# Optimization experiments

Measured on AMD Instinct MI355X. Metric: run time of the kernel, lower is better.

## Reference

```python
import jax, jax.numpy as jnp
import numpy as np

B, T, R, V = 16, 512, 128, 64
HOURS = 24.0


def setup_inputs() -> dict:
    key = jax.random.key(0)
    k1, k2, k3, k4, k5 = jax.random.split(key, 5)
    x = jax.random.normal(k1, (B, T, V), dtype=jnp.float32)
    # observation mask in {0,1}
    m = (jax.random.uniform(k2, (B, T, V)) < 0.5).astype(jnp.float32)
    # irregular observation times in [0, HOURS), sorted per sample
    t = jnp.sort(jax.random.uniform(k3, (B, T), dtype=jnp.float32) * HOURS, axis=1)
    # hold-out mask (only used in reconstruction branch; kept for signature parity)
    h = (jax.random.uniform(k4, (B, T, V)) < 0.5).astype(jnp.float32)
    # learnable per-variable kernel bandwidth (pre-softplus), shape (1,1,1,V)
    kernel = jax.random.normal(k5, (1, 1, 1, V), dtype=jnp.float32) * 0.1
    # fixed reference time grid, shape (R,)
    ref_t = jnp.linspace(0.0, HOURS, R, dtype=jnp.float32)
    return {"x": x, "m": m, "t": t, "h": h, "kernel": kernel, "ref_t": ref_t}


def reference(x, m, t, h, kernel, ref_t):
    # squared time distances: (B, T, R)
    d2 = (t[:, :, None] - ref_t[None, None, :]) ** 2
    pos_kernel = jnp.log1p(jnp.exp(kernel))          # softplus, (1,1,1,V)
    w = pos_kernel * d2[:, :, :, None]               # (B, T, R, V)
    m4 = m[:, :, None, :]                            # (B, T, 1, V)
    x4 = x[:, :, None, :]
    # low-pass branch
    w_lp = jnp.exp(-w) * m4
    lambda_ = w_lp.sum(axis=1)                       # (B, R, V)
    sigma = (w_lp * x4).sum(axis=1) / jnp.maximum(lambda_, 1.0)
    # high-pass branch
    w_hp = jnp.exp(-10.0 * w) * m4
    lambda_hp = w_hp.sum(axis=1)
    gamma = (w_hp * x4).sum(axis=1) / jnp.maximum(lambda_hp, 1.0)
    return (sigma, lambda_, gamma)
```

## Files before the change

kernel.cpp:

```cpp
#include <hip/hip_runtime.h>
#include <hip/hip_bf16.h>

#define NB 16
#define NT 512
#define NR 128
#define NV 64
#define RG 4
#define NCH 8

__global__ __launch_bounds__(512) void interp_kernel(
    const float* __restrict__ x,
    const float* __restrict__ m,
    const float* __restrict__ t,
    const float* __restrict__ kern,
    const float* __restrict__ ref_t,
    float* __restrict__ out)
{
    __shared__ float ts[NT];
    __shared__ float red[NCH][4 * RG][NV];

    const int tid   = threadIdx.x;
    const int v     = tid & 63;
    const int chunk = tid >> 6;
    const int bid   = blockIdx.x;
    const int b     = bid >> 5;
    const int rg    = bid & 31;
    const int r0    = rg * RG;

    for (int i = tid; i < NT; i += 512) ts[i] = t[b * NT + i];

    const float kv  = kern[v];
    const float pk  = log1pf(__expf(kv));
    const float npk = -pk;

    float rt[RG];
#pragma unroll
    for (int j = 0; j < RG; ++j) rt[j] = ref_t[r0 + j];

    float lam[RG], sig[RG], lamh[RG], gam[RG];
#pragma unroll
    for (int j = 0; j < RG; ++j) { lam[j] = 0.f; sig[j] = 0.f; lamh[j] = 0.f; gam[j] = 0.f; }

    __syncthreads();

    const int t_base = chunk * (NT / NCH);
    const float* __restrict__ xrow = x + (size_t)b * NT * NV + v;
    const float* __restrict__ mrow = m + (size_t)b * NT * NV + v;

    for (int i = 0; i < NT / NCH; ++i) {
        const int tt   = t_base + i;
        const float tv = ts[tt];
        const float mv = mrow[(size_t)tt * NV];
        const float xv = xrow[(size_t)tt * NV];
        const float mx = mv * xv;
#pragma unroll
        for (int j = 0; j < RG; ++j) {
            const float dt  = tv - rt[j];
            const float wn  = npk * (dt * dt);
            const float e   = __expf(wn);
            const float e10 = __expf(10.0f * wn);
            lam[j]  = fmaf(e,   mv, lam[j]);
            sig[j]  = fmaf(e,   mx, sig[j]);
            lamh[j] = fmaf(e10, mv, lamh[j]);
            gam[j]  = fmaf(e10, mx, gam[j]);
        }
    }

#pragma unroll
    for (int j = 0; j < RG; ++j) {
        red[chunk][j * 4 + 0][v] = lam[j];
        red[chunk][j * 4 + 1][v] = sig[j];
        red[chunk][j * 4 + 2][v] = lamh[j];
        red[chunk][j * 4 + 3][v] = gam[j];
    }
    __syncthreads();

    if (chunk < RG) {
        const int jj = chunk;
        float flam = 0.f, fsig = 0.f, flamh = 0.f, fgam = 0.f;
#pragma unroll
        for (int c = 0; c < NCH; ++c) {
            flam  += red[c][jj * 4 + 0][v];
            fsig  += red[c][jj * 4 + 1][v];
            flamh += red[c][jj * 4 + 2][v];
            fgam  += red[c][jj * 4 + 3][v];
        }
        const float sigma = fsig / fmaxf(flam, 1.0f);
        const float gamma = fgam / fmaxf(flamh, 1.0f);

        const int r = r0 + jj;
        const size_t o = ((size_t)b * NR + r) * NV + v;
        out[o]                            = sigma;
        out[o + (size_t)NB * NR * NV]     = flam;
        out[o + (size_t)2 * NB * NR * NV] = gamma;
    }
}

extern "C" void kernel_launch(void* const* d_in, const int* in_sizes, int n_in,
                              void* d_out, int out_size, void* d_ws, size_t ws_size,
                              hipStream_t stream) {
    const float* x     = (const float*)d_in[0];
    const float* m     = (const float*)d_in[1];
    const float* t     = (const float*)d_in[2];
    const float* kern  = (const float*)d_in[4];
    const float* ref_t = (const float*)d_in[5];
    float* out = (float*)d_out;

    dim3 grid(NB * (NR / RG));
    dim3 block(512);
    interp_kernel<<<grid, block, 0, stream>>>(x, m, t, kern, ref_t, out);
}
```

Baseline: 89.70 us.

## Restrict time loop to window around reference points via binary search cutoff

```diff
diff --git a/kernel.cpp b/kernel.cpp
--- a/kernel.cpp
+++ b/kernel.cpp
@@ -1,5 +1,4 @@
 #include <hip/hip_runtime.h>
-#include <hip/hip_bf16.h>
 
 #define NB 16
 #define NT 512
@@ -7,6 +6,8 @@
 #define NV 64
 #define RG 4
 #define NCH 8
+
+#define CUT 12.0f
 
 __global__ __launch_bounds__(512) void interp_kernel(
     const float* __restrict__ x,
@@ -27,15 +28,23 @@
     const int rg    = bid & 31;
     const int r0    = rg * RG;
 
-    for (int i = tid; i < NT; i += 512) ts[i] = t[b * NT + i];
+    ts[tid] = t[b * NT + tid];
 
-    const float kv  = kern[v];
-    const float pk  = log1pf(__expf(kv));
-    const float npk = -pk;
+    const float kv   = kern[v];
+    const float pk   = log1pf(__expf(kv));
+    const float npk2 = -pk * 1.44269504088896f;
+
+    float pmin = pk;
+#pragma unroll
+    for (int off = 1; off < 64; off <<= 1)
+        pmin = fminf(pmin, __shfl_xor(pmin, off));
+    const float dmax = __fsqrt_rn(CUT / pmin);
 
     float rt[RG];
 #pragma unroll
     for (int j = 0; j < RG; ++j) rt[j] = ref_t[r0 + j];
+    const float wlo = rt[0]      - dmax;
+    const float whi = rt[RG - 1] + dmax;
 
     float lam[RG], sig[RG], lamh[RG], gam[RG];
 #pragma unroll
@@ -43,22 +52,30 @@
 
     __syncthreads();
 
-    const int t_base = chunk * (NT / NCH);
+    int lo, hi;
+    {
+        int l = 0, r = NT;
+        while (l < r) { int mid = (l + r) >> 1; if (ts[mid] < wlo) l = mid + 1; else r = mid; }
+        lo = l;
+        l = 0; r = NT;
+        while (l < r) { int mid = (l + r) >> 1; if (ts[mid] <= whi) l = mid + 1; else r = mid; }
+        hi = l;
+    }
+
     const float* __restrict__ xrow = x + (size_t)b * NT * NV + v;
     const float* __restrict__ mrow = m + (size_t)b * NT * NV + v;
 
-    for (int i = 0; i < NT / NCH; ++i) {
-        const int tt   = t_base + i;
-        const float tv = ts[tt];
-        const float mv = mrow[(size_t)tt * NV];
-        const float xv = xrow[(size_t)tt * NV];
+    for (int i = lo + chunk; i < hi; i += NCH) {
+        const float tv = ts[i];
+        const float mv = mrow[(size_t)i * NV];
+        const float xv = xrow[(size_t)i * NV];
         const float mx = mv * xv;
 #pragma unroll
         for (int j = 0; j < RG; ++j) {
             const float dt  = tv - rt[j];
-            const float wn  = npk * (dt * dt);
-            const float e   = __expf(wn);
-            const float e10 = __expf(10.0f * wn);
+            const float wn2 = npk2 * (dt * dt);
+            const float e   = exp2f(wn2);
+            const float e10 = exp2f(10.0f * wn2);
             lam[j]  = fmaf(e,   mv, lam[j]);
             sig[j]  = fmaf(e,   mx, sig[j]);
             lamh[j] = fmaf(e10, mv, lamh[j]);
```

Result: faster. 84.94 us (-5.3%).
